# Kernel tuning notes

Measured on AMD Instinct MI355X. Metric: run time of the kernel, lower is better.

Reference implementation:

```python
import jax, jax.numpy as jnp
import numpy as np

B, V, NFEAT, INTER, NHID1, NHID12, NCLASS = 131072, 8, 32, 8, 16, 8, 2


def setup_inputs() -> dict:
    key = jax.random.key(0)
    ks = jax.random.split(key, 16)
    # node feature tensor: channel 0 = node type in {0,1}, channels 1..32 = features
    types = jax.random.randint(ks[0], (B, V, 1), 0, 2).astype(jnp.float32)
    feats = jax.random.normal(ks[1], (B, V, NFEAT), dtype=jnp.float32)
    x = jnp.concatenate([types, feats], axis=-1)  # (B, V, 33)
    adj = jax.random.uniform(ks[2], (B, V, V), dtype=jnp.float32)
    edge_attr = jax.random.normal(ks[3], (B, V, V), dtype=jnp.float32)
    s = lambda k, *sh: jax.random.normal(k, sh, dtype=jnp.float32) * 0.1
    return {
        "x": x, "adj": adj, "edge_attr": edge_attr,
        "wa": s(ks[4], INTER, NFEAT), "ba": jnp.zeros((INTER,), jnp.float32),
        "wb": s(ks[5], INTER, NFEAT), "bb": jnp.zeros((INTER,), jnp.float32),
        "w1": s(ks[6], NFEAT, NHID1), "b1": jnp.zeros((NHID1,), jnp.float32),
        "w2": s(ks[7], NHID1, NHID12), "b2": jnp.zeros((NHID12,), jnp.float32),
        "wg": s(ks[8], NHID12, NHID12), "bg": jnp.zeros((NHID12,), jnp.float32),
        "wf": s(ks[9], NCLASS, NHID12), "bf": jnp.zeros((NCLASS,), jnp.float32),
    }


def _attn_pool(h, wg, bg):
    # GlobalAttentionPooling: softmax(gate_nn(h)) over nodes, weighted sum
    gate = jax.nn.softmax(jnp.einsum('bvc,oc->bvo', h, wg) + bg, axis=1)
    return jnp.sum(gate * h, axis=1)  # (B, NHID12)


def reference(x, adj, edge_attr, wa, ba, wb, bb, w1, b1, w2, b2, wg, bg, wf, bf):
    node_types = x[..., 0]           # (B, V)
    feat = x[..., 1:]                # (B, V, 32)
    # conv_b (1x1 conv == per-node linear), output layout (B, inter, V)
    Fk = jnp.einsum('bvc,oc->bov', feat, wb) + bb[None, :, None]  # (B, 8, V=8)
    S = jax.nn.softmax(jnp.matmul(Fk, Fk), axis=1)                # (B, 8, 8)
    W = adj * (S + edge_attr)                                     # (B, V, V)
    # graph conv 1: (W @ feat) @ w1 + b1, LeakyReLU(0.01)
    h = jax.nn.leaky_relu(jnp.einsum('bvw,bwc->bvc', W, feat) @ w1 + b1)
    # graph conv 2
    h = jax.nn.leaky_relu(jnp.einsum('bvw,bwc->bvc', W, h) @ w2 + b2)  # (B, V, 8)
    # per-type masked attention pooling; types fixed to {0, 1}
    pooled = []
    for t in (0.0, 1.0):
        mask = (node_types == t)[..., None].astype(h.dtype)
        pooled.append(_attn_pool(h * mask, wg, bg))
    x_pool = jnp.mean(jnp.stack(pooled, axis=1), axis=1)  # (B, NHID12)
    return x_pool @ wf.T + bf  # (B, NCLASS)
```

## Files before the change

kernel.cpp:

```cpp
#include <hip/hip_runtime.h>


#define SLOTS 16
#define NTHREADS 128

typedef float v2f __attribute__((ext_vector_type(2)));
typedef float4 __attribute__((aligned(4))) f4u;

#define WBT 0
#define W1O 256
#define W2O 768
#define WGT 896
#define BBO 960
#define B1O 968
#define B2O 984
#define NWF 992

__device__ __forceinline__ float grp_sum8(float x) {
    x += __shfl_xor(x, 1);
    x += __shfl_xor(x, 2);
    x += __shfl_xor(x, 4);
    return x;
}
__device__ __forceinline__ void wavefence() { __builtin_amdgcn_wave_barrier(); }
__device__ __forceinline__ v2f mkv(float a, float b) { v2f r; r.x = a; r.y = b; return r; }

__global__ __launch_bounds__(NTHREADS, 4)
void gcn_fused(const float* __restrict__ x,
               const float* __restrict__ adj,
               const float* __restrict__ edge,
               const float* __restrict__ wb, const float* __restrict__ bb,
               const float* __restrict__ w1, const float* __restrict__ b1,
               const float* __restrict__ w2, const float* __restrict__ b2,
               const float* __restrict__ wg, const float* __restrict__ bg,
               const float* __restrict__ wf, const float* __restrict__ bf,
               float* __restrict__ out, int nGroups)
{
    __shared__ float bufA[SLOTS * 72];
    __shared__ float bufB[SLOTS * 136];
    __shared__ float wS[NWF];

    const int tid  = threadIdx.x;
    const int slot = tid >> 3;
    const int v    = tid & 7;
    float* A  = &bufA[slot * 72];
    float* Bg = &bufB[slot * 136];

    {
        for (int i = tid; i < 256; i += NTHREADS) {
            const int c = i >> 3, o = i & 7;
            wS[WBT + i] = wb[o * 32 + c];
        }
        for (int i = tid; i < 512; i += NTHREADS) wS[W1O + i] = w1[i];
        if (tid < 128) wS[W2O + tid] = w2[tid];
        if (tid < 64) {
            const int n = tid >> 3, o = tid & 7;
            wS[WGT + tid] = wg[o * 8 + n];
        }
        if (tid < 8)  wS[BBO + tid] = bb[tid];
        if (tid < 16) wS[B1O + tid] = b1[tid];
        if (tid < 8)  wS[B2O + tid] = b2[tid];
    }
    __syncthreads();

    long long bb_ = (long long)blockIdx.x * SLOTS + slot;
    if (bb_ >= (long long)nGroups * SLOTS) bb_ = (long long)nGroups * SLOTS - 1;
    const size_t b = (size_t)bb_;

    const float* xr = x + b * 264 + (size_t)v * 33;
    const float type = xr[0];
    const f4u* xq = (const f4u*)(xr + 1);
    float4 q[8];
#pragma unroll
    for (int k = 0; k < 8; ++k) q[k] = xq[k];

    v2f Fk2[4];
    {
        const v2f* bbp = (const v2f*)&wS[BBO];
#pragma unroll
        for (int p = 0; p < 4; ++p) Fk2[p] = bbp[p];
    }
    v2f g12[8];
#pragma unroll
    for (int p = 0; p < 8; ++p) g12[p] = mkv(0.f, 0.f);
#pragma unroll
    for (int k = 0; k < 8; ++k) {
        const float f[4] = { q[k].x, q[k].y, q[k].z, q[k].w };
#pragma unroll
        for (int u = 0; u < 4; ++u) {
            const int c = 4 * k + u;
            const v2f f2 = mkv(f[u], f[u]);
            const float4* wbc = (const float4*)&wS[WBT + c * 8];
            const float4 wa = wbc[0], wbq = wbc[1];
            Fk2[0] = __builtin_elementwise_fma(f2, mkv(wa.x,  wa.y),  Fk2[0]);
            Fk2[1] = __builtin_elementwise_fma(f2, mkv(wa.z,  wa.w),  Fk2[1]);
            Fk2[2] = __builtin_elementwise_fma(f2, mkv(wbq.x, wbq.y), Fk2[2]);
            Fk2[3] = __builtin_elementwise_fma(f2, mkv(wbq.z, wbq.w), Fk2[3]);
            const float4* w1c = (const float4*)&wS[W1O + c * 16];
            const float4 wc0 = w1c[0], wc1 = w1c[1], wc2 = w1c[2], wc3 = w1c[3];
            g12[0] = __builtin_elementwise_fma(f2, mkv(wc0.x, wc0.y), g12[0]);
            g12[1] = __builtin_elementwise_fma(f2, mkv(wc0.z, wc0.w), g12[1]);
            g12[2] = __builtin_elementwise_fma(f2, mkv(wc1.x, wc1.y), g12[2]);
            g12[3] = __builtin_elementwise_fma(f2, mkv(wc1.z, wc1.w), g12[3]);
            g12[4] = __builtin_elementwise_fma(f2, mkv(wc2.x, wc2.y), g12[4]);
            g12[5] = __builtin_elementwise_fma(f2, mkv(wc2.z, wc2.w), g12[5]);
            g12[6] = __builtin_elementwise_fma(f2, mkv(wc3.x, wc3.y), g12[6]);
            g12[7] = __builtin_elementwise_fma(f2, mkv(wc3.z, wc3.w), g12[7]);
        }
    }

    const float4* ar = (const float4*)(adj  + b * 64 + (size_t)v * 8);
    const float4* er = (const float4*)(edge + b * 64 + (size_t)v * 8);
    const float4 a0 = ar[0], a1 = ar[1];
    const float4 e0 = er[0], e1 = er[1];

#pragma unroll
    for (int p = 0; p < 4; ++p) {
        A[(2 * p)     * 8 + v] = Fk2[p].x;
        A[(2 * p + 1) * 8 + v] = Fk2[p].y;
    }
    {
        float4* gp = (float4*)(Bg + v * 16);
        gp[0] = make_float4(g12[0].x, g12[0].y, g12[1].x, g12[1].y);
        gp[1] = make_float4(g12[2].x, g12[2].y, g12[3].x, g12[3].y);
        gp[2] = make_float4(g12[4].x, g12[4].y, g12[5].x, g12[5].y);
        gp[3] = make_float4(g12[6].x, g12[6].y, g12[7].x, g12[7].y);
    }
    wavefence();

    float M[8];
#pragma unroll
    for (int o = 0; o < 8; ++o) {
        const float4* fr = (const float4*)(A + o * 8);
        const float4 r0 = fr[0], r1 = fr[1];
        v2f acc = mkv(0.f, 0.f);
        acc = __builtin_elementwise_fma(mkv(r0.x, r0.y), Fk2[0], acc);
        acc = __builtin_elementwise_fma(mkv(r0.z, r0.w), Fk2[1], acc);
        acc = __builtin_elementwise_fma(mkv(r1.x, r1.y), Fk2[2], acc);
        acc = __builtin_elementwise_fma(mkv(r1.z, r1.w), Fk2[3], acc);
        M[o] = acc.x + acc.y;
    }
    wavefence();
    float mx = M[0];
#pragma unroll
    for (int o = 1; o < 8; ++o) mx = fmaxf(mx, M[o]);
    float ssum = 0.f;
#pragma unroll
    for (int o = 0; o < 8; ++o) { M[o] = __expf(M[o] - mx); ssum += M[o]; }
    const float sinv = 1.f / ssum;
#pragma unroll
    for (int o = 0; o < 8; ++o) A[o * 8 + v] = M[o] * sinv;
    wavefence();

    const float4* sr = (const float4*)(A + v * 8);
    const float4 s0 = sr[0], s1 = sr[1];
    v2f W2[4];
    W2[0] = mkv(a0.x, a0.y) * (mkv(s0.x, s0.y) + mkv(e0.x, e0.y));
    W2[1] = mkv(a0.z, a0.w) * (mkv(s0.z, s0.w) + mkv(e0.z, e0.w));
    W2[2] = mkv(a1.x, a1.y) * (mkv(s1.x, s1.y) + mkv(e1.x, e1.y));
    W2[3] = mkv(a1.z, a1.w) * (mkv(s1.z, s1.w) + mkv(e1.z, e1.w));

    v2f m1[8];
#pragma unroll
    for (int p = 0; p < 8; ++p) m1[p] = mkv(0.f, 0.f);
#pragma unroll
    for (int w = 0; w < 8; ++w) {
        const float wv = (w & 1) ? W2[w >> 1].y : W2[w >> 1].x;
        const v2f f2 = mkv(wv, wv);
        const float4* gp = (const float4*)(Bg + w * 16);
        const float4 q0 = gp[0], q1 = gp[1], q2 = gp[2], q3 = gp[3];
        m1[0] = __builtin_elementwise_fma(f2, mkv(q0.x, q0.y), m1[0]);
        m1[1] = __builtin_elementwise_fma(f2, mkv(q0.z, q0.w), m1[1]);
        m1[2] = __builtin_elementwise_fma(f2, mkv(q1.x, q1.y), m1[2]);
        m1[3] = __builtin_elementwise_fma(f2, mkv(q1.z, q1.w), m1[3]);
        m1[4] = __builtin_elementwise_fma(f2, mkv(q2.x, q2.y), m1[4]);
        m1[5] = __builtin_elementwise_fma(f2, mkv(q2.z, q2.w), m1[5]);
        m1[6] = __builtin_elementwise_fma(f2, mkv(q3.x, q3.y), m1[6]);
        m1[7] = __builtin_elementwise_fma(f2, mkv(q3.z, q3.w), m1[7]);
    }
    v2f h[8];
    {
        const v2f* b1p = (const v2f*)&wS[B1O];
        const v2f k01 = mkv(0.01f, 0.01f);
#pragma unroll
        for (int p = 0; p < 8; ++p) {
            const v2f t = m1[p] + b1p[p];
            h[p] = __builtin_elementwise_max(t, t * k01);
        }
    }

    v2f g22[4];
#pragma unroll
    for (int p = 0; p < 4; ++p) g22[p] = mkv(0.f, 0.f);
#pragma unroll
    for (int j = 0; j < 16; ++j) {
        const float hv = (j & 1) ? h[j >> 1].y : h[j >> 1].x;
        const v2f f2 = mkv(hv, hv);
        const float4* w2r = (const float4*)&wS[W2O + j * 8];
        const float4 r0 = w2r[0], r1 = w2r[1];
        g22[0] = __builtin_elementwise_fma(f2, mkv(r0.x, r0.y), g22[0]);
        g22[1] = __builtin_elementwise_fma(f2, mkv(r0.z, r0.w), g22[1]);
        g22[2] = __builtin_elementwise_fma(f2, mkv(r1.x, r1.y), g22[2]);
        g22[3] = __builtin_elementwise_fma(f2, mkv(r1.z, r1.w), g22[3]);
    }
    wavefence();
    {
        float4* gp = (float4*)(A + v * 8);
        gp[0] = make_float4(g22[0].x, g22[0].y, g22[1].x, g22[1].y);
        gp[1] = make_float4(g22[2].x, g22[2].y, g22[3].x, g22[3].y);
    }
    wavefence();

    v2f m2[4];
#pragma unroll
    for (int p = 0; p < 4; ++p) m2[p] = mkv(0.f, 0.f);
#pragma unroll
    for (int w = 0; w < 8; ++w) {
        const float wv = (w & 1) ? W2[w >> 1].y : W2[w >> 1].x;
        const v2f f2 = mkv(wv, wv);
        const float4* gp = (const float4*)(A + w * 8);
        const float4 q0 = gp[0], q1 = gp[1];
        m2[0] = __builtin_elementwise_fma(f2, mkv(q0.x, q0.y), m2[0]);
        m2[1] = __builtin_elementwise_fma(f2, mkv(q0.z, q0.w), m2[1]);
        m2[2] = __builtin_elementwise_fma(f2, mkv(q1.x, q1.y), m2[2]);
        m2[3] = __builtin_elementwise_fma(f2, mkv(q1.z, q1.w), m2[3]);
    }
    v2f h2[4];
    {
        const v2f* b2p = (const v2f*)&wS[B2O];
        const v2f k01 = mkv(0.01f, 0.01f);
#pragma unroll
        for (int p = 0; p < 4; ++p) {
            const v2f t = m2[p] + b2p[p];
            h2[p] = __builtin_elementwise_max(t, t * k01);
        }
    }

    v2f Y2[4];
#pragma unroll
    for (int p = 0; p < 4; ++p) Y2[p] = mkv(0.f, 0.f);
#pragma unroll
    for (int n = 0; n < 8; ++n) {
        const float hv = (n & 1) ? h2[n >> 1].y : h2[n >> 1].x;
        const v2f f2 = mkv(hv, hv);
        const float4* wgr = (const float4*)&wS[WGT + n * 8];
        const float4 r0 = wgr[0], r1 = wgr[1];
        Y2[0] = __builtin_elementwise_fma(f2, mkv(r0.x, r0.y), Y2[0]);
        Y2[1] = __builtin_elementwise_fma(f2, mkv(r0.z, r0.w), Y2[1]);
        Y2[2] = __builtin_elementwise_fma(f2, mkv(r1.x, r1.y), Y2[2]);
        Y2[3] = __builtin_elementwise_fma(f2, mkv(r1.z, r1.w), Y2[3]);
    }
    wavefence();
    {
        float4* hp = (float4*)(A + v * 8);
        hp[0] = make_float4(h2[0].x, h2[0].y, h2[1].x, h2[1].y);
        hp[1] = make_float4(h2[2].x, h2[2].y, h2[3].x, h2[3].y);
        float4* yp = (float4*)(Bg + v * 8);
        yp[0] = make_float4(Y2[0].x, Y2[0].y, Y2[1].x, Y2[1].y);
        yp[1] = make_float4(Y2[2].x, Y2[2].y, Y2[3].x, Y2[3].y);
        Bg[64 + v] = type;
    }
    wavefence();

    const int o = v;
    float yc[8], hc[8], ty[8];
#pragma unroll
    for (int vp = 0; vp < 8; ++vp) {
        yc[vp] = Bg[vp * 8 + o];
        hc[vp] = A[vp * 8 + o];
        ty[vp] = Bg[64 + vp];
    }
    float xp = 0.f;
#pragma unroll
    for (int t = 0; t < 2; ++t) {
        const float tv = (float)t;
        float l[8];
        float lmx = -1e30f;
#pragma unroll
        for (int vp = 0; vp < 8; ++vp) {
            l[vp] = (ty[vp] == tv) ? yc[vp] : 0.f;
            lmx = fmaxf(lmx, l[vp]);
        }
        float esum = 0.f, num = 0.f;
#pragma unroll
        for (int vp = 0; vp < 8; ++vp) {
            const float e = __expf(l[vp] - lmx);
            esum += e;
            num  += (ty[vp] == tv) ? e * hc[vp] : 0.f;
        }
        xp += 0.5f * num / esum;
    }

    const float y0 = grp_sum8(xp * wf[0 * 8 + o]);
    const float y1 = grp_sum8(xp * wf[1 * 8 + o]);
    if (v == 0) {
        float2* op = (float2*)(out + b * 2);
        *op = make_float2(y0 + bf[0], y1 + bf[1]);
    }
}

extern "C" void kernel_launch(void* const* d_in, const int* in_sizes, int n_in,
                              void* d_out, int out_size, void* d_ws, size_t ws_size,
                              hipStream_t stream) {
    const float* x    = (const float*)d_in[0];
    const float* adj  = (const float*)d_in[1];
    const float* edge = (const float*)d_in[2];
    const float* wb   = (const float*)d_in[5];
    const float* bb   = (const float*)d_in[6];
    const float* w1   = (const float*)d_in[7];
    const float* b1   = (const float*)d_in[8];
    const float* w2   = (const float*)d_in[9];
    const float* b2   = (const float*)d_in[10];
    const float* wg   = (const float*)d_in[11];
    const float* bg   = (const float*)d_in[12];
    const float* wf   = (const float*)d_in[13];
    const float* bf   = (const float*)d_in[14];
    float* out = (float*)d_out;

    const int Btot    = in_sizes[0] / 264;
    const int nGroups = (Btot + SLOTS - 1) / SLOTS;

    gcn_fused<<<nGroups, NTHREADS, 0, stream>>>(x, adj, edge, wb, bb, w1, b1,
                                                w2, b2, wg, bg, wf, bf, out, nGroups);
}
```

Baseline: 275.7 us.

## Coalesce node-feature loads via swizzled LDS staging and hoist adj/edge loads

Node features are now read cooperatively: in each load, lanes of a slot fetch consecutive float4 chunks of the same node row. The chunks are written to a per-slot LDS tile with a rotating swizzle to avoid bank conflicts, then read back in per-node order for the projection loop. This replaces the earlier scheme where each thread read its own 33-float row with a wide stride. The adj and edge loads are issued earlier so their latency overlaps the feature staging. The shared buffers are merged into one array, so the staging tile aliases the later A/Bg buffers. This costs extra LDS traffic, a slightly larger LDS footprint and extra wave barriers.

```diff
diff --git a/kernel.cpp b/kernel.cpp
--- a/kernel.cpp
+++ b/kernel.cpp
@@ -36,43 +36,55 @@
                const float* __restrict__ wf, const float* __restrict__ bf,
                float* __restrict__ out, int nGroups)
 {
-    __shared__ float bufA[SLOTS * 72];
-    __shared__ float bufB[SLOTS * 136];
-    __shared__ float wS[NWF];
+    __shared__ float lds[4096 + NWF];
 
     const int tid  = threadIdx.x;
     const int slot = tid >> 3;
     const int v    = tid & 7;
-    float* A  = &bufA[slot * 72];
-    float* Bg = &bufB[slot * 136];
-
-    {
-        for (int i = tid; i < 256; i += NTHREADS) {
-            const int c = i >> 3, o = i & 7;
-            wS[WBT + i] = wb[o * 32 + c];
-        }
-        for (int i = tid; i < 512; i += NTHREADS) wS[W1O + i] = w1[i];
-        if (tid < 128) wS[W2O + tid] = w2[tid];
-        if (tid < 64) {
-            const int n = tid >> 3, o = tid & 7;
-            wS[WGT + tid] = wg[o * 8 + n];
-        }
-        if (tid < 8)  wS[BBO + tid] = bb[tid];
-        if (tid < 16) wS[B1O + tid] = b1[tid];
-        if (tid < 8)  wS[B2O + tid] = b2[tid];
-    }
+    const int sl   = slot & 7;
+    const int wavebase = (slot >> 3) * 2048;
+    float* xW = &lds[wavebase + sl * 256];
+    float* A  = &lds[wavebase + sl * 72];
+    float* Bg = &lds[wavebase + 576 + sl * 136];
+    float* wS = &lds[4096];
+
+    for (int i = tid; i < 256; i += NTHREADS) {
+        const int o = i >> 5, c = i & 31;
+        wS[WBT + c * 8 + o] = wb[i];
+    }
+    for (int i = tid; i < 512; i += NTHREADS) wS[W1O + i] = w1[i];
+    if (tid < 128) wS[W2O + tid] = w2[tid];
+    if (tid < 64) {
+        const int o = tid >> 3, n = tid & 7;
+        wS[WGT + n * 8 + o] = wg[tid];
+    }
+    if (tid < 8)  wS[BBO + tid] = bb[tid];
+    if (tid < 16) wS[B1O + tid] = b1[tid];
+    if (tid < 8)  wS[B2O + tid] = b2[tid];
     __syncthreads();
 
     long long bb_ = (long long)blockIdx.x * SLOTS + slot;
     if (bb_ >= (long long)nGroups * SLOTS) bb_ = (long long)nGroups * SLOTS - 1;
     const size_t b = (size_t)bb_;
 
-    const float* xr = x + b * 264 + (size_t)v * 33;
-    const float type = xr[0];
-    const f4u* xq = (const f4u*)(xr + 1);
-    float4 q[8];
-#pragma unroll
-    for (int k = 0; k < 8; ++k) q[k] = xq[k];
+    const float4* ar = (const float4*)(adj  + b * 64 + (size_t)v * 8);
+    const float4* er = (const float4*)(edge + b * 64 + (size_t)v * 8);
+    const float4 a0 = ar[0], a1 = ar[1];
+    const float4 e0 = er[0], e1 = er[1];
+
+    const float* xb = x + b * 264;
+    const float type = xb[v * 33];
+    float4 xf[8];
+#pragma unroll
+    for (int n = 0; n < 8; ++n)
+        xf[n] = *(const f4u*)(xb + n * 33 + 1 + v * 4);
+
+#pragma unroll
+    for (int n = 0; n < 8; ++n)
+        *(float4*)(xW + n * 32 + (((v + n + sl) & 7) << 2)) = xf[n];
+    wavefence();
+
+    const int K0 = (v + sl) & 7;
 
     v2f Fk2[4];
     {
@@ -85,7 +97,8 @@
     for (int p = 0; p < 8; ++p) g12[p] = mkv(0.f, 0.f);
 #pragma unroll
     for (int k = 0; k < 8; ++k) {
-        const float f[4] = { q[k].x, q[k].y, q[k].z, q[k].w };
+        const float4 qk = *(const float4*)(xW + v * 32 + (((k + K0) & 7) << 2));
+        const float f[4] = { qk.x, qk.y, qk.z, qk.w };
 #pragma unroll
         for (int u = 0; u < 4; ++u) {
             const int c = 4 * k + u;
@@ -108,11 +121,7 @@
             g12[7] = __builtin_elementwise_fma(f2, mkv(wc3.z, wc3.w), g12[7]);
         }
     }
-
-    const float4* ar = (const float4*)(adj  + b * 64 + (size_t)v * 8);
-    const float4* er = (const float4*)(edge + b * 64 + (size_t)v * 8);
-    const float4 a0 = ar[0], a1 = ar[1];
-    const float4 e0 = er[0], e1 = er[1];
+    wavefence();
 
 #pragma unroll
     for (int p = 0; p < 4; ++p) {
```

Result: faster. 269.2 us (-2.4%).
